# Kernel optimization log

Hardware: AMD Instinct MI355X
Metric: run time of the kernel (lower is better)

## Reference

```python
import jax, jax.numpy as jnp
import numpy as np
from jax import lax

H = 64
X = 128
T = 8192
A_SCALE = 0.1
A_IDENTITY = 0.9


def setup_inputs() -> dict:
    key = jax.random.key(0)
    k1, k2, k3, k4 = jax.random.split(key, 4)
    x_seq = jax.random.normal(k1, (T, X), dtype=jnp.float32)
    h0 = jax.random.normal(k2, (H,), dtype=jnp.float32)
    # orthogonal-ish init for A_raw (exact orthogonality not required for correctness)
    A_raw = jnp.linalg.qr(jax.random.normal(k3, (H, H), dtype=jnp.float32))[0]
    B = jax.random.normal(k4, (H, X), dtype=jnp.float32) * (1.0 / np.sqrt(X))
    c = jnp.zeros((H,), dtype=jnp.float32)
    return {"x_seq": x_seq, "h0": h0, "A_raw": A_raw, "B": B, "c": c}


def reference(x_seq, h0, A_raw, B, c):
    # A = a_identity * I + a_scale * A_raw  (fixed dense transition matrix)
    A = A_IDENTITY * jnp.eye(H, dtype=x_seq.dtype) + A_SCALE * A_raw
    # b_t = B x_t + c, kept as column vectors [T, H, 1]
    b_seq = (x_seq @ B.T + c[None, :])[..., None]
    A_seq = jnp.broadcast_to(A, (T, H, H))

    def combine(left, right):
        A1, b1 = left
        A2, b2 = right
        return (A2 @ A1, A2 @ b1 + b2)

    A_pref, b_pref = lax.associative_scan(combine, (A_seq, b_seq), axis=0)
    b_pref = b_pref[..., 0]                 # [T, H]
    h_all = A_pref @ h0 + b_pref            # [T, H]
    return h_all
```

## Files before the change

kernel.cpp:

```cpp
#include <hip/hip_runtime.h>
#include <hip/hip_bf16.h>

#define T_ 8192
#define H_ 64
#define X_ 128
#define C_ 128
#define L_ 64
#define TB 8

__device__ __forceinline__ float bcast(float v, int src) {
    return __int_as_float(__builtin_amdgcn_readlane(__float_as_int(v), src));
}

__device__ __forceinline__ float lru_step(const float* arow, float h, float b_i) {
    float a0 = b_i, a1 = 0.f, a2 = 0.f, a3 = 0.f;
#pragma unroll
    for (int j = 0; j < 16; ++j) {
        a0 = fmaf(arow[j],      bcast(h, j),      a0);
        a1 = fmaf(arow[j + 16], bcast(h, j + 16), a1);
        a2 = fmaf(arow[j + 32], bcast(h, j + 32), a2);
        a3 = fmaf(arow[j + 48], bcast(h, j + 48), a3);
    }
    return (a0 + a1) + (a2 + a3);
}

__device__ __forceinline__ void load_arow_A(const float* __restrict__ A_raw,
                                            int lane, float* arow) {
    const float4* a4 = (const float4*)(A_raw + lane * 64);
#pragma unroll
    for (int q = 0; q < 16; ++q) {
        float4 t4 = a4[q];
        arow[4 * q + 0] = 0.1f * t4.x;
        arow[4 * q + 1] = 0.1f * t4.y;
        arow[4 * q + 2] = 0.1f * t4.z;
        arow[4 * q + 3] = 0.1f * t4.w;
    }
#pragma unroll
    for (int q = 0; q < 64; ++q) arow[q] += (q == lane) ? 0.9f : 0.0f;
}

__global__ __launch_bounds__(256) void k_bproj(const float* __restrict__ x,
                                               const float* __restrict__ B,
                                               const float* __restrict__ c,
                                               float* __restrict__ b_out) {
    __shared__ float Bs[H_][X_ + 1];
    __shared__ float xs[TB][X_];
    const int tid = threadIdx.x;
    const int t0 = blockIdx.x * TB;

    for (int idx = tid; idx < H_ * X_; idx += 256) {
        Bs[idx >> 7][idx & 127] = B[idx];
    }
    for (int idx = tid; idx < TB * X_; idx += 256) {
        xs[idx >> 7][idx & 127] = x[t0 * X_ + idx];
    }
    __syncthreads();

    const int h  = tid & 63;
    const int tp = tid >> 6;
    const float cc = c[h];
    float acc0 = cc, acc1 = cc;
#pragma unroll 4
    for (int xx = 0; xx < X_; ++xx) {
        const float bv = Bs[h][xx];
        acc0 = fmaf(xs[tp][xx],     bv, acc0);
        acc1 = fmaf(xs[tp + 4][xx], bv, acc1);
    }
    b_out[(size_t)(t0 + tp) * H_ + h]     = acc0;
    b_out[(size_t)(t0 + tp + 4) * H_ + h] = acc1;
}

__global__ __launch_bounds__(64) void k_phase1(const float* __restrict__ A_raw,
                                               const float* __restrict__ b,
                                               float* __restrict__ v,
                                               float* __restrict__ AL) {
    const int lane = threadIdx.x;
    const int wid  = blockIdx.x;
    float arow[64];
    load_arow_A(A_raw, lane, arow);

    if (wid < C_) {
        const float* bc = b + (size_t)wid * L_ * H_;
        float h = 0.f;
#pragma unroll 2
        for (int t = 0; t < L_; ++t) {
            const float bi = bc[(size_t)t * H_ + lane];
            h = lru_step(arow, h, bi);
        }
        v[wid * H_ + lane] = h;
    } else {
        const int col = wid - C_;
        float h = (lane == col) ? 1.f : 0.f;
#pragma unroll 2
        for (int t = 0; t < L_; ++t) {
            h = lru_step(arow, h, 0.f);
        }
        AL[lane * 64 + col] = h;
    }
}

__global__ __launch_bounds__(64) void k_phase2(const float* __restrict__ AL,
                                               const float* __restrict__ h0,
                                               const float* __restrict__ v,
                                               float* __restrict__ hstart) {
    const int lane = threadIdx.x;
    float arow[64];
    const float4* a4 = (const float4*)(AL + lane * 64);
#pragma unroll
    for (int q = 0; q < 16; ++q) {
        float4 t4 = a4[q];
        arow[4 * q + 0] = t4.x;
        arow[4 * q + 1] = t4.y;
        arow[4 * q + 2] = t4.z;
        arow[4 * q + 3] = t4.w;
    }
    float h = h0[lane];
#pragma unroll 2
    for (int c = 0; c < C_; ++c) {
        hstart[c * H_ + lane] = h;
        const float vi = v[c * H_ + lane];
        h = lru_step(arow, h, vi);
    }
}

__global__ __launch_bounds__(64) void k_phase3(const float* __restrict__ A_raw,
                                               const float* __restrict__ hstart,
                                               float* __restrict__ out) {
    const int lane = threadIdx.x;
    const int cid  = blockIdx.x;
    float arow[64];
    load_arow_A(A_raw, lane, arow);

    float h = hstart[cid * H_ + lane];
    float* oc = out + (size_t)cid * L_ * H_;
#pragma unroll 2
    for (int t = 0; t < L_; ++t) {
        const float bi = oc[(size_t)t * H_ + lane];
        h = lru_step(arow, h, bi);
        oc[(size_t)t * H_ + lane] = h;
    }
}

extern "C" void kernel_launch(void* const* d_in, const int* in_sizes, int n_in,
                              void* d_out, int out_size, void* d_ws, size_t ws_size,
                              hipStream_t stream) {
    const float* x     = (const float*)d_in[0];
    const float* h0    = (const float*)d_in[1];
    const float* A_raw = (const float*)d_in[2];
    const float* B     = (const float*)d_in[3];
    const float* c     = (const float*)d_in[4];
    float* out = (float*)d_out;
    float* ws  = (float*)d_ws;

    float* AL     = ws;
    float* v      = ws + 4096;
    float* hstart = ws + 4096 + 8192;

    k_bproj <<<T_ / TB, 256, 0, stream>>>(x, B, c, out);
    k_phase1<<<C_ + H_, 64, 0, stream>>>(A_raw, out, v, AL);
    k_phase2<<<1,       64, 0, stream>>>(AL, h0, v, hstart);
    k_phase3<<<C_,      64, 0, stream>>>(A_raw, hstart, out);
}
```

Before: 88.81 us.

## Broadcast recurrent state via LDS and rewrite B-projection without shared staging

The per-step matvec now broadcasts the hidden state through a double-buffered LDS array with float4 reads, where before it used 64 readlane instructions per step. The next bias value is prefetched one step ahead in the three scan kernels. The B-projection kernel drops its shared-memory staging: each wave reads B rows and x rows directly from global memory with float4 loads and computes four timesteps per lane, giving sixteen timesteps per block. The cost is a __syncthreads on every step in the serial chain, and the projection now relies on caches to reuse B.

Result: slower. 114.6 us (+29.1%).

```diff
diff --git a/kernel.cpp b/kernel.cpp
--- a/kernel.cpp
+++ b/kernel.cpp
@@ -6,27 +6,28 @@
 #define X_ 128
 #define C_ 128
 #define L_ 64
-#define TB 8
+#define K1_TB 16
 
-__device__ __forceinline__ float bcast(float v, int src) {
-    return __int_as_float(__builtin_amdgcn_readlane(__float_as_int(v), src));
-}
-
-__device__ __forceinline__ float lru_step(const float* arow, float h, float b_i) {
+__device__ __forceinline__ float lru_step_lds(const float* arow, float h, float b_i,
+                                              float* hsbuf, int lane) {
+    hsbuf[lane] = h;
+    __syncthreads();
+    const float4* h4 = (const float4*)hsbuf;
     float a0 = b_i, a1 = 0.f, a2 = 0.f, a3 = 0.f;
 #pragma unroll
-    for (int j = 0; j < 16; ++j) {
-        a0 = fmaf(arow[j],      bcast(h, j),      a0);
-        a1 = fmaf(arow[j + 16], bcast(h, j + 16), a1);
-        a2 = fmaf(arow[j + 32], bcast(h, j + 32), a2);
-        a3 = fmaf(arow[j + 48], bcast(h, j + 48), a3);
+    for (int q = 0; q < 16; ++q) {
+        float4 hv = h4[q];
+        a0 = fmaf(arow[4 * q + 0], hv.x, a0);
+        a1 = fmaf(arow[4 * q + 1], hv.y, a1);
+        a2 = fmaf(arow[4 * q + 2], hv.z, a2);
+        a3 = fmaf(arow[4 * q + 3], hv.w, a3);
     }
     return (a0 + a1) + (a2 + a3);
 }
 
 __device__ __forceinline__ void load_arow_A(const float* __restrict__ A_raw,
                                             int lane, float* arow) {
-    const float4* a4 = (const float4*)(A_raw + lane * 64);
+    const float4* a4 = (const float4*)(A_raw + lane * H_);
 #pragma unroll
     for (int q = 0; q < 16; ++q) {
         float4 t4 = a4[q];
@@ -43,49 +44,60 @@
                                                const float* __restrict__ B,
                                                const float* __restrict__ c,
                                                float* __restrict__ b_out) {
-    __shared__ float Bs[H_][X_ + 1];
-    __shared__ float xs[TB][X_];
-    const int tid = threadIdx.x;
-    const int t0 = blockIdx.x * TB;
+    const int lane = threadIdx.x & 63;
+    const int w    = __builtin_amdgcn_readfirstlane(threadIdx.x >> 6);
+    const int t0   = blockIdx.x * K1_TB + w * 4;
 
-    for (int idx = tid; idx < H_ * X_; idx += 256) {
-        Bs[idx >> 7][idx & 127] = B[idx];
+    const float cc = c[lane];
+    float acc[4];
+#pragma unroll
+    for (int r = 0; r < 4; ++r) acc[r] = cc;
+
+    const float* Brow = B + lane * X_;
+#pragma unroll
+    for (int kc = 0; kc < 4; ++kc) {
+        float4 br[8];
+        const float4* b4 = (const float4*)(Brow + kc * 32);
+#pragma unroll
+        for (int q = 0; q < 8; ++q) br[q] = b4[q];
+#pragma unroll
+        for (int r = 0; r < 4; ++r) {
+            const float4* xr = (const float4*)(x + (size_t)(t0 + r) * X_ + kc * 32);
+#pragma unroll
+            for (int q = 0; q < 8; ++q) {
+                float4 xv = xr[q];
+                acc[r] = fmaf(br[q].x, xv.x, acc[r]);
+                acc[r] = fmaf(br[q].y, xv.y, acc[r]);
+                acc[r] = fmaf(br[q].z, xv.z, acc[r]);
+                acc[r] = fmaf(br[q].w, xv.w, acc[r]);
+            }
+        }
     }
-    for (int idx = tid; idx < TB * X_; idx += 256) {
-        xs[idx >> 7][idx & 127] = x[t0 * X_ + idx];
+#pragma unroll
+    for (int r = 0; r < 4; ++r) {
+        b_out[(size_t)(t0 + r) * H_ + lane] = acc[r];
     }
-    __syncthreads();
-
-    const int h  = tid & 63;
-    const int tp = tid >> 6;
-    const float cc = c[h];
-    float acc0 = cc, acc1 = cc;
-#pragma unroll 4
-    for (int xx = 0; xx < X_; ++xx) {
-        const float bv = Bs[h][xx];
-        acc0 = fmaf(xs[tp][xx],     bv, acc0);
-        acc1 = fmaf(xs[tp + 4][xx], bv, acc1);
-    }
-    b_out[(size_t)(t0 + tp) * H_ + h]     = acc0;
-    b_out[(size_t)(t0 + tp + 4) * H_ + h] = acc1;
 }
 
 __global__ __launch_bounds__(64) void k_phase1(const float* __restrict__ A_raw,
                                                const float* __restrict__ b,
                                                float* __restrict__ v,
                                                float* __restrict__ AL) {
+    __shared__ __align__(16) float hs[2][H_];
     const int lane = threadIdx.x;
     const int wid  = blockIdx.x;
     float arow[64];
     load_arow_A(A_raw, lane, arow);
 
     if (wid < C_) {
-        const float* bc = b + (size_t)wid * L_ * H_;
+        const float* bc = b + (size_t)wid * L_ * H_ + lane;
         float h = 0.f;
+        float bnext = bc[0];
 #pragma unroll 2
         for (int t = 0; t < L_; ++t) {
-            const float bi = bc[(size_t)t * H_ + lane];
-            h = lru_step(arow, h, bi);
+            const float bi = bnext;
+            if (t + 1 < L_) bnext = bc[(size_t)(t + 1) * H_];
+            h = lru_step_lds(arow, h, bi, hs[t & 1], lane);
         }
         v[wid * H_ + lane] = h;
     } else {
@@ -93,9 +105,9 @@
         float h = (lane == col) ? 1.f : 0.f;
 #pragma unroll 2
         for (int t = 0; t < L_; ++t) {
-            h = lru_step(arow, h, 0.f);
+            h = lru_step_lds(arow, h, 0.f, hs[t & 1], lane);
         }
-        AL[lane * 64 + col] = h;
+        AL[lane * H_ + col] = h;
     }
 }
 
@@ -103,9 +115,10 @@
                                                const float* __restrict__ h0,
                                                const float* __restrict__ v,
                                                float* __restrict__ hstart) {
+    __shared__ __align__(16) float hs[2][H_];
     const int lane = threadIdx.x;
     float arow[64];
-    const float4* a4 = (const float4*)(AL + lane * 64);
+    const float4* a4 = (const float4*)(AL + lane * H_);
 #pragma unroll
     for (int q = 0; q < 16; ++q) {
         float4 t4 = a4[q];
@@ -115,29 +128,34 @@
         arow[4 * q + 3] = t4.w;
     }
     float h = h0[lane];
+    float vnext = v[lane];
 #pragma unroll 2
     for (int c = 0; c < C_; ++c) {
         hstart[c * H_ + lane] = h;
-        const float vi = v[c * H_ + lane];
-        h = lru_step(arow, h, vi);
+        const float vi = vnext;
+        if (c + 1 < C_) vnext = v[(c + 1) * H_ + lane];
+        h = lru_step_lds(arow, h, vi, hs[c & 1], lane);
     }
 }
 
 __global__ __launch_bounds__(64) void k_phase3(const float* __restrict__ A_raw,
                                                const float* __restrict__ hstart,
                                                float* __restrict__ out) {
+    __shared__ __align__(16) float hs[2][H_];
     const int lane = threadIdx.x;
     const int cid  = blockIdx.x;
     float arow[64];
     load_arow_A(A_raw, lane, arow);
 
     float h = hstart[cid * H_ + lane];
-    float* oc = out + (size_t)cid * L_ * H_;
+    float* oc = out + (size_t)cid * L_ * H_ + lane;
+    float bnext = oc[0];
 #pragma unroll 2
     for (int t = 0; t < L_; ++t) {
-        const float bi = oc[(size_t)t * H_ + lane];
-        h = lru_step(arow, h, bi);
-        oc[(size_t)t * H_ + lane] = h;
+        const float bi = bnext;
+        if (t + 1 < L_) bnext = oc[(size_t)(t + 1) * H_];
+        h = lru_step_lds(arow, h, bi, hs[t & 1], lane);
+        oc[(size_t)t * H_] = h;
     }
 }
 
@@ -156,8 +174,8 @@
     float* v      = ws + 4096;
     float* hstart = ws + 4096 + 8192;
 
-    k_bproj <<<T_ / TB, 256, 0, stream>>>(x, B, c, out);
-    k_phase1<<<C_ + H_, 64, 0, stream>>>(A_raw, out, v, AL);
-    k_phase2<<<1,       64, 0, stream>>>(AL, h0, v, hstart);
-    k_phase3<<<C_,      64, 0, stream>>>(A_raw, hstart, out);
+    k_bproj <<<T_ / K1_TB, 256, 0, stream>>>(x, B, c, out);
+    k_phase1<<<C_ + H_,    64,  0, stream>>>(A_raw, out, v, AL);
+    k_phase2<<<1,          64,  0, stream>>>(AL, h0, v, hstart);
+    k_phase3<<<C_,         64,  0, stream>>>(A_raw, hstart, out);
 }
```
